# Kernel tuning notes

Hardware: AMD Instinct MI355X
Metric: run time of the kernel (lower is better)

Reference implementation:

```python
import jax, jax.numpy as jnp
import numpy as np

N_NODES = 50000
N_EDGES = 1600000
F_IN = 128
C = 64          # block in/out channels
EF = 64         # edge MLP hidden dim
BLOCKS = 3
MLP_DIM = 128
N_CLASSES = 10
N_GRAPHS = 512
EPS = 1e-5


def setup_inputs() -> dict:
    key = jax.random.key(0)
    ks = jax.random.split(key, 32)
    s = 0.05
    inp = {
        "x": jax.random.normal(ks[0], (N_NODES, F_IN), jnp.float32),
        "edge_index": jax.random.randint(ks[1], (2, N_EDGES), 0, N_NODES, jnp.int64),
        "batch": jnp.sort(jax.random.randint(ks[2], (N_NODES,), 0, N_GRAPHS, jnp.int64)),
        "fc0_w": jax.random.normal(ks[3], (F_IN, C), jnp.float32) * s,
        "fc0_b": jnp.zeros((C,), jnp.float32),
        "fc1_w": jax.random.normal(ks[4], (BLOCKS * C, MLP_DIM), jnp.float32) * s,
        "fc1_b": jnp.zeros((MLP_DIM,), jnp.float32),
        "fc2_w": jax.random.normal(ks[5], (MLP_DIM, N_CLASSES), jnp.float32) * s,
        "fc2_b": jnp.zeros((N_CLASSES,), jnp.float32),
    }
    for i in range(BLOCKS):
        k = 6 + 4 * i
        inp[f"bn_g{i}"] = jnp.ones((C,), jnp.float32)
        inp[f"bn_b{i}"] = jnp.zeros((C,), jnp.float32)
        inp[f"w1_{i}"] = jax.random.normal(ks[k], (2 * C, EF), jnp.float32) * s
        inp[f"b1_{i}"] = jnp.zeros((EF,), jnp.float32)
        inp[f"w2_{i}"] = jax.random.normal(ks[k + 1], (EF, C), jnp.float32) * s
        inp[f"b2_{i}"] = jnp.zeros((C,), jnp.float32)
    return inp


def _batchnorm(x, g, b):
    mu = jnp.mean(x, axis=0)
    var = jnp.var(x, axis=0)
    return (x - mu) * jax.lax.rsqrt(var + EPS) * g + b


def _edge_conv(x, src, dst, w1, b1, w2, b2):
    # PyG-style EdgeConv: msg = MLP(concat[x_i, x_j - x_i]), max-aggregate at i
    xi = x[dst]                                  # [E, C]
    xj = x[src]                                  # [E, C]
    h = jax.nn.relu(jnp.concatenate([xi, xj - xi], axis=-1) @ w1 + b1)  # [E, EF]
    m = h @ w2 + b2                              # [E, C]
    agg = jax.ops.segment_max(m, dst, num_segments=N_NODES)
    return jnp.where(jnp.isfinite(agg), agg, 0.0)


def reference(x, edge_index, batch, fc0_w, fc0_b, fc1_w, fc1_b, fc2_w, fc2_b,
              bn_g0, bn_b0, w1_0, b1_0, w2_0, b2_0,
              bn_g1, bn_b1, w1_1, b1_1, w2_1, b2_1,
              bn_g2, bn_b2, w1_2, b1_2, w2_2, b2_2):
    src, dst = edge_index[0], edge_index[1]
    h = x @ fc0_w + fc0_b                        # [N, C]
    blocks = [(bn_g0, bn_b0, w1_0, b1_0, w2_0, b2_0),
              (bn_g1, bn_b1, w1_1, b1_1, w2_1, b2_1),
              (bn_g2, bn_b2, w1_2, b1_2, w2_2, b2_2)]
    xs = []
    for (g, b, w1, b1, w2, b2) in blocks:
        h = _batchnorm(h, g, b)
        h = jax.nn.relu(_edge_conv(h, src, dst, w1, b1, w2, b2))
        xs.append(h)
    cat = jnp.concatenate(xs, axis=-1)           # [N, 3C]
    # global mean pool over graphs
    sums = jax.ops.segment_sum(cat, batch, num_segments=N_GRAPHS)
    cnt = jax.ops.segment_sum(jnp.ones((N_NODES,), cat.dtype), batch,
                              num_segments=N_GRAPHS)
    pooled = sums / jnp.maximum(cnt, 1.0)[:, None]   # [G, 3C]
    hid = jax.nn.relu(pooled @ fc1_w + fc1_b)
    return jax.nn.log_softmax(hid @ fc2_w + fc2_b, axis=-1)
```

## Files before the change

kernel.cpp:

```cpp
#include <hip/hip_runtime.h>
#include <math.h>

#define N_NODES 50000
#define N_TILES 3125
#define N_EDGES 1600000
#define F_IN 128
#define C 64
#define EF 64
#define N_GRAPHS 512
#define MLP_DIM 128
#define N_CLASSES 10
#define EPS 1e-5f
#define NB 196
#define CAPB 16384
#define CHUNK 4096
#define NPASS1 391
#define NFC0 782
#define NSLICE 8

typedef __attribute__((ext_vector_type(8))) _Float16 half8;
typedef __attribute__((ext_vector_type(2))) _Float16 half2v;
typedef __attribute__((ext_vector_type(4))) float floatx4;
typedef __attribute__((ext_vector_type(4))) unsigned uintx4;

union Uh { uintx4 v; half2v h[4]; half8 h8; };

__device__ __forceinline__ unsigned short f2h(float a) {
    union { _Float16 f; unsigned short u; } c;
    c.f = (_Float16)a;
    return c.u;
}
__device__ __forceinline__ float h2f(unsigned short u) {
    union { unsigned short u; _Float16 f; } c;
    c.u = u;
    return (float)c.f;
}
__device__ __forceinline__ half2v pk2(float a, float b) {
    auto t = __builtin_amdgcn_cvt_pkrtz(a, b);
    union { decltype(t) i; half2v o; } c;
    c.i = t;
    return c.o;
}

__global__ __launch_bounds__(256, 3) void fc0_pass1_kernel(
        const int* __restrict__ src, const int* __restrict__ dst,
        int* __restrict__ gcur, unsigned* __restrict__ keys,
        const float* __restrict__ x, const float* __restrict__ w,
        const float* __restrict__ b, unsigned short* __restrict__ h0,
        float* __restrict__ bns) {
    __shared__ int lcnt[NB], lbase[NB], lcnt2[NB];
    __shared__ float bl1[4][64], bl2[4][64];
    int tid = threadIdx.x;

    if (blockIdx.x < NPASS1) {
        int e0 = blockIdx.x * CHUNK;
        unsigned k[CHUNK / 256];
        int bk[CHUNK / 256];
        for (int i = tid; i < NB; i += 256) lcnt[i] = 0;
        __syncthreads();
#pragma unroll
        for (int i = 0; i < CHUNK / 256; i++) {
            int e = e0 + i * 256 + tid;
            if (e < N_EDGES) {
                int d = dst[e];
                k[i] = ((unsigned)d << 16) | (unsigned)src[e];
                bk[i] = d >> 8;
                atomicAdd(&lcnt[bk[i]], 1);
            } else bk[i] = -1;
        }
        __syncthreads();
        for (int i = tid; i < NB; i += 256) {
            int c = lcnt[i];
            lbase[i] = c ? atomicAdd(&gcur[i], c) : 0;
            lcnt2[i] = 0;
        }
        __syncthreads();
#pragma unroll
        for (int i = 0; i < CHUNK / 256; i++) {
            if (bk[i] >= 0) {
                int r = atomicAdd(&lcnt2[bk[i]], 1);
                keys[(size_t)bk[i] * CAPB + lbase[bk[i]] + r] = k[i];
            }
        }
        return;
    }

    int bid = blockIdx.x - NPASS1;
    int lane = tid & 63, wid = tid >> 6;
    int q = lane >> 4, cl = lane & 15, kq = q * 8;

    Uh wf[4][4];
#pragma unroll
    for (int kh = 0; kh < 4; kh++)
#pragma unroll
        for (int cb = 0; cb < 4; cb++)
#pragma unroll
            for (int j = 0; j < 4; j++) {
                int k0 = kh * 32 + kq + 2 * j;
                int col = cb * 16 + cl;
                wf[kh][cb].h[j] = pk2(w[k0 * 64 + col], w[(k0 + 1) * 64 + col]);
            }
    float bv[4];
#pragma unroll
    for (int cb = 0; cb < 4; cb++) bv[cb] = b[cb * 16 + cl];
    float s1[4] = {0, 0, 0, 0}, s2[4] = {0, 0, 0, 0};

    for (int t = bid * 4 + wid; t < N_TILES; t += NFC0 * 4) {
        int nb = t * 16;
        floatx4 acc[4] = {{0,0,0,0},{0,0,0,0},{0,0,0,0},{0,0,0,0}};
#pragma unroll
        for (int kh = 0; kh < 4; kh++) {
            const float* xr = x + (size_t)(nb + cl) * F_IN + kh * 32 + kq;
            floatx4 xa = *(const floatx4*)xr;
            floatx4 xb = *(const floatx4*)(xr + 4);
            Uh xf;
            xf.h[0] = pk2(xa.x, xa.y); xf.h[1] = pk2(xa.z, xa.w);
            xf.h[2] = pk2(xb.x, xb.y); xf.h[3] = pk2(xb.z, xb.w);
#pragma unroll
            for (int cb = 0; cb < 4; cb++)
                acc[cb] = __builtin_amdgcn_mfma_f32_16x16x32_f16(xf.h8, wf[kh][cb].h8, acc[cb], 0, 0, 0);
        }
#pragma unroll
        for (int cb = 0; cb < 4; cb++)
#pragma unroll
            for (int r = 0; r < 4; r++) {
                float v = acc[cb][r] + bv[cb];
                h0[(size_t)(nb + q * 4 + r) * 64 + cb * 16 + cl] = f2h(v);
                s1[cb] += v; s2[cb] += v * v;
            }
    }
#pragma unroll
    for (int cb = 0; cb < 4; cb++) {
        s1[cb] += __shfl_xor(s1[cb], 16); s1[cb] += __shfl_xor(s1[cb], 32);
        s2[cb] += __shfl_xor(s2[cb], 16); s2[cb] += __shfl_xor(s2[cb], 32);
    }
    if (lane < 16) {
#pragma unroll
        for (int cb = 0; cb < 4; cb++) { bl1[wid][cb * 16 + lane] = s1[cb]; bl2[wid][cb * 16 + lane] = s2[cb]; }
    }
    __syncthreads();
    if (tid < 64) {
        float a  = bl1[0][tid] + bl1[1][tid] + bl1[2][tid] + bl1[3][tid];
        float c2 = bl2[0][tid] + bl2[1][tid] + bl2[2][tid] + bl2[3][tid];
        int sl = bid & (NSLICE - 1);
        atomicAdd(&bns[sl * 128 + tid], a);
        atomicAdd(&bns[sl * 128 + 64 + tid], c2);
    }
}

__device__ __forceinline__ void ab_body(int bid, int tid,
                                        const unsigned short* __restrict__ h,
                                        const float* __restrict__ bns,
                                        const float* __restrict__ g,
                                        const float* __restrict__ bb,
                                        const float* __restrict__ w1,
                                        const float* __restrict__ b1,
                                        unsigned short* __restrict__ A,
                                        unsigned short* __restrict__ Bb,
                                        float* scale, float* shift, float* cab) {
    int lane = tid & 63, wid = tid >> 6;
    int q = lane >> 4, cl = lane & 15, kq = q * 8;

    if (tid < 64) {
        float s1v = 0.f, s2v = 0.f;
#pragma unroll
        for (int s = 0; s < NSLICE; s++) { s1v += bns[s * 128 + tid]; s2v += bns[s * 128 + 64 + tid]; }
        float mu  = s1v * (1.0f / N_NODES);
        float var = s2v * (1.0f / N_NODES) - mu * mu;
        float sc  = g[tid] * rsqrtf(var + EPS);
        scale[tid] = sc;
        shift[tid] = bb[tid] - mu * sc;
    }
    __syncthreads();
    if (tid < 128) {
        int j = tid & 63;
        float acc = (tid < 64) ? b1[j] : 0.f;
        for (int k = 0; k < 64; k++) {
            float wa_ = w1[k * EF + j], wb_ = w1[(64 + k) * EF + j];
            acc = fmaf(shift[k], (tid < 64) ? (wa_ - wb_) : wb_, acc);
        }
        cab[tid] = acc;
    }
    Uh wa[2][4], wb[2][4];
#pragma unroll
    for (int kh = 0; kh < 2; kh++)
#pragma unroll
        for (int cb = 0; cb < 4; cb++)
#pragma unroll
            for (int j = 0; j < 4; j++) {
                int k0 = kh * 32 + kq + 2 * j;
                int col = cb * 16 + cl;
                float sa = scale[k0], sb = scale[k0 + 1];
                float a0 = w1[k0 * EF + col], b0 = w1[(64 + k0) * EF + col];
                float a1 = w1[(k0 + 1) * EF + col], b1v = w1[(64 + k0 + 1) * EF + col];
                wa[kh][cb].h[j] = pk2(sa * (a0 - b0), sb * (a1 - b1v));
                wb[kh][cb].h[j] = pk2(sa * b0, sb * b1v);
            }
    __syncthreads();
    float cav[4], cbv[4];
#pragma unroll
    for (int cb = 0; cb < 4; cb++) { cav[cb] = cab[cb * 16 + cl]; cbv[cb] = cab[64 + cb * 16 + cl]; }

    for (int t = bid * 4 + wid; t < N_TILES; t += NFC0 * 4) {
        int nb = t * 16;
        const unsigned short* hrow = h + (size_t)(nb + cl) * 64 + kq;
        Uh h0f, h1f;
        h0f.v = *(const uintx4*)hrow;
        h1f.v = *(const uintx4*)(hrow + 32);
        floatx4 accA[4] = {{0,0,0,0},{0,0,0,0},{0,0,0,0},{0,0,0,0}};
        floatx4 accB[4] = {{0,0,0,0},{0,0,0,0},{0,0,0,0},{0,0,0,0}};
#pragma unroll
        for (int cb = 0; cb < 4; cb++) {
            accA[cb] = __builtin_amdgcn_mfma_f32_16x16x32_f16(h0f.h8, wa[0][cb].h8, accA[cb], 0, 0, 0);
            accB[cb] = __builtin_amdgcn_mfma_f32_16x16x32_f16(h0f.h8, wb[0][cb].h8, accB[cb], 0, 0, 0);
            accA[cb] = __builtin_amdgcn_mfma_f32_16x16x32_f16(h1f.h8, wa[1][cb].h8, accA[cb], 0, 0, 0);
            accB[cb] = __builtin_amdgcn_mfma_f32_16x16x32_f16(h1f.h8, wb[1][cb].h8, accB[cb], 0, 0, 0);
        }
#pragma unroll
        for (int cb = 0; cb < 4; cb++)
#pragma unroll
            for (int r = 0; r < 4; r++) {
                size_t o = (size_t)(nb + q * 4 + r) * 64 + cb * 16 + cl;
                A[o]  = f2h(accA[cb][r] + cav[cb]);
                Bb[o] = f2h(accB[cb][r] + cbv[cb]);
            }
    }
}

__global__ __launch_bounds__(256, 4) void sort2_ab_kernel(
        const unsigned* __restrict__ keys, const int* __restrict__ bcnt,
        int* __restrict__ cnt, int* __restrict__ gtotal,
        int* __restrict__ row_start, unsigned short* __restrict__ sorted_src,
        const unsigned short* __restrict__ h, const float* __restrict__ bns,
        const float* __restrict__ g, const float* __restrict__ bb,
        const float* __restrict__ w1, const float* __restrict__ b1,
        unsigned short* __restrict__ A, unsigned short* __restrict__ Bb) {
    __shared__ int lc[256], loc[256], rs[256], cur[256];
    __shared__ int base;
    __shared__ float scale[64], shift[64], cab[128];
    int tid = threadIdx.x;
    if (blockIdx.x < NB) {
        int b = blockIdx.x;
        lc[tid] = 0;
        cur[tid] = 0;
        __syncthreads();
        int beg = b * CAPB, end = beg + bcnt[b];
        const unsigned* kb = keys + beg;
        int nk = end - beg;
        for (int p = tid; p < nk; p += 256)
            atomicAdd(&lc[(kb[p] >> 16) & 255], 1);
        __syncthreads();
        int node = b * 256 + tid;
        int c = lc[tid];
        if (node < N_NODES) cnt[node] = c;
        int pc = (c + 15) & ~15;
        loc[tid] = pc;
        __syncthreads();
        for (int off = 1; off < 256; off <<= 1) {
            int t = (tid >= off) ? loc[tid - off] : 0;
            __syncthreads();
            loc[tid] += t;
            __syncthreads();
        }
        if (tid == 255) base = atomicAdd(gtotal, loc[255]);
        __syncthreads();
        int myrs = base + loc[tid] - pc;
        rs[tid] = myrs;
        if (node < N_NODES) row_start[node] = myrs;
        __syncthreads();
        for (int p = tid; p < nk; p += 256) {
            unsigned k = kb[p];
            int lidx = (k >> 16) & 255;
            int r = atomicAdd(&cur[lidx], 1);
            sorted_src[rs[lidx] + r] = (unsigned short)(k & 0xFFFFu);
        }
        __syncthreads();
        if (node < N_NODES && c > 0) {
            unsigned short s0 = sorted_src[myrs];
            int pe = myrs + pc;
            for (int p = myrs + c; p < pe; p++) sorted_src[p] = s0;
        }
        return;
    }
    ab_body(blockIdx.x - NB, tid, h, bns, g, bb, w1, b1, A, Bb, scale, shift, cab);
}

__global__ __launch_bounds__(256, 4) void ab_mfma_kernel(
        const unsigned short* __restrict__ h, const float* __restrict__ bns,
        const float* __restrict__ g, const float* __restrict__ bb,
        const float* __restrict__ w1, const float* __restrict__ b1,
        unsigned short* __restrict__ A, unsigned short* __restrict__ Bb) {
    __shared__ float scale[64], shift[64], cab[128];
    ab_body(blockIdx.x, threadIdx.x, h, bns, g, bb, w1, b1, A, Bb, scale, shift, cab);
}

__global__ __launch_bounds__(256, 4) void edge_mfma_kernel(
        const unsigned short* __restrict__ A, const unsigned short* __restrict__ Bb,
        const int* __restrict__ row_start, const int* __restrict__ cnt,
        const unsigned short* __restrict__ sorted_src,
        const float* __restrict__ w2, const float* __restrict__ b2,
        unsigned short* __restrict__ catp, float* __restrict__ bnsNext) {
    __shared__ float r1[4][64], r2[4][64];
    int tid = threadIdx.x, lane = tid & 63, wid = tid >> 6;
    int kq = (lane >> 4) * 8;
    int cl = lane & 15;

    Uh bfr[2][4];
#pragma unroll
    for (int kh = 0; kh < 2; kh++)
#pragma unroll
        for (int cb = 0; cb < 4; cb++)
#pragma unroll
            for (int j = 0; j < 4; j++) {
                _Float16 w0 = (_Float16)w2[(kh * 32 + kq + 2 * j) * 64 + cb * 16 + cl];
                _Float16 w1 = (_Float16)w2[(kh * 32 + kq + 2 * j + 1) * 64 + cb * 16 + cl];
                bfr[kh][cb].h[j] = half2v{w0, w1};
            }
    float b2j = b2[lane];
    float s1 = 0.f, s2 = 0.f;
    const half2v zeroh = {(_Float16)0.f, (_Float16)0.f};

    for (int n = blockIdx.x * 4 + wid; n < N_NODES; n += gridDim.x * 4) {
        int beg = row_start[n];
        int end = beg + ((cnt[n] + 15) & ~15);
        const unsigned short* arow = A + (size_t)n * 64 + kq;
        Uh a0u, a1u;
        a0u.v = *(const uintx4*)(arow);
        a1u.v = *(const uintx4*)(arow + 32);
        floatx4 rmax0 = {-INFINITY, -INFINITY, -INFINITY, -INFINITY};
        floatx4 rmax1 = rmax0, rmax2 = rmax0, rmax3 = rmax0;

        auto tile = [&](uintx4 u0, uintx4 u1) {
            Uh b0u, b1u, f0, f1;
            b0u.v = u0; b1u.v = u1;
#pragma unroll
            for (int j = 0; j < 4; j++) {
                f0.h[j] = __builtin_elementwise_max(a0u.h[j] + b0u.h[j], zeroh);
                f1.h[j] = __builtin_elementwise_max(a1u.h[j] + b1u.h[j], zeroh);
            }
            floatx4 acc0 = {0.f, 0.f, 0.f, 0.f}, acc1 = acc0, acc2 = acc0, acc3 = acc0;
            acc0 = __builtin_amdgcn_mfma_f32_16x16x32_f16(f0.h8, bfr[0][0].h8, acc0, 0, 0, 0);
            acc1 = __builtin_amdgcn_mfma_f32_16x16x32_f16(f0.h8, bfr[0][1].h8, acc1, 0, 0, 0);
            acc2 = __builtin_amdgcn_mfma_f32_16x16x32_f16(f0.h8, bfr[0][2].h8, acc2, 0, 0, 0);
            acc3 = __builtin_amdgcn_mfma_f32_16x16x32_f16(f0.h8, bfr[0][3].h8, acc3, 0, 0, 0);
            acc0 = __builtin_amdgcn_mfma_f32_16x16x32_f16(f1.h8, bfr[1][0].h8, acc0, 0, 0, 0);
            acc1 = __builtin_amdgcn_mfma_f32_16x16x32_f16(f1.h8, bfr[1][1].h8, acc1, 0, 0, 0);
            acc2 = __builtin_amdgcn_mfma_f32_16x16x32_f16(f1.h8, bfr[1][2].h8, acc2, 0, 0, 0);
            acc3 = __builtin_amdgcn_mfma_f32_16x16x32_f16(f1.h8, bfr[1][3].h8, acc3, 0, 0, 0);
            rmax0 = __builtin_elementwise_max(rmax0, acc0);
            rmax1 = __builtin_elementwise_max(rmax1, acc1);
            rmax2 = __builtin_elementwise_max(rmax2, acc2);
            rmax3 = __builtin_elementwise_max(rmax3, acc3);
        };
        auto gather = [&](int p, uintx4& u0, uintx4& u1) {
            int srcm = sorted_src[p + cl];
            const unsigned short* brow = Bb + (size_t)srcm * 64 + kq;
            u0 = *(const uintx4*)(brow);
            u1 = *(const uintx4*)(brow + 32);
        };

        int p0 = beg;
        for (; p0 + 32 <= end; p0 += 32) {
            uintx4 x0, x1, y0, y1;
            gather(p0, x0, x1);
            gather(p0 + 16, y0, y1);
            tile(x0, x1);
            tile(y0, y1);
        }
        if (p0 < end) {
            uintx4 x0, x1;
            gather(p0, x0, x1);
            tile(x0, x1);
        }

        float v0 = fmaxf(fmaxf(rmax0.x, rmax0.y), fmaxf(rmax0.z, rmax0.w));
        float v1 = fmaxf(fmaxf(rmax1.x, rmax1.y), fmaxf(rmax1.z, rmax1.w));
        float v2 = fmaxf(fmaxf(rmax2.x, rmax2.y), fmaxf(rmax2.z, rmax2.w));
        float v3 = fmaxf(fmaxf(rmax3.x, rmax3.y), fmaxf(rmax3.z, rmax3.w));
        v0 = fmaxf(v0, __shfl_xor(v0, 16)); v0 = fmaxf(v0, __shfl_xor(v0, 32));
        v1 = fmaxf(v1, __shfl_xor(v1, 16)); v1 = fmaxf(v1, __shfl_xor(v1, 32));
        v2 = fmaxf(v2, __shfl_xor(v2, 16)); v2 = fmaxf(v2, __shfl_xor(v2, 32));
        v3 = fmaxf(v3, __shfl_xor(v3, 16)); v3 = fmaxf(v3, __shfl_xor(v3, 32));
        float vs = (lane & 32) ? ((lane & 16) ? v3 : v2) : ((lane & 16) ? v1 : v0);
        float v = fmaxf(vs + b2j, 0.f);
        catp[(size_t)n * 64 + lane] = f2h(v);
        s1 += v; s2 += v * v;
    }

    if (bnsNext) {
        r1[wid][lane] = s1; r2[wid][lane] = s2;
        __syncthreads();
        if (tid < 64) {
            float a  = r1[0][tid] + r1[1][tid] + r1[2][tid] + r1[3][tid];
            float c2 = r2[0][tid] + r2[1][tid] + r2[2][tid] + r2[3][tid];
            int sl = blockIdx.x & (NSLICE - 1);
            atomicAdd(&bnsNext[sl * 128 + tid], a);
            atomicAdd(&bnsNext[sl * 128 + 64 + tid], c2);
        }
    }
}

__global__ __launch_bounds__(192) void poolhead_kernel(const unsigned short* __restrict__ cat0,
                                                       const unsigned short* __restrict__ cat1,
                                                       const unsigned short* __restrict__ cat2,
                                                       const int* __restrict__ batch,
                                                       const float* __restrict__ fc1w,
                                                       const float* __restrict__ fc1b,
                                                       const float* __restrict__ fc2w,
                                                       const float* __restrict__ fc2b,
                                                       float* __restrict__ out) {
    __shared__ int se[2];
    __shared__ float p[192];
    __shared__ float hid[128];
    __shared__ float z[10];
    __shared__ float lse;
    int g = blockIdx.x, tid = threadIdx.x;
    if (tid < 2) {
        int target = g + tid;
        int lo = 0, hi = N_NODES;
        while (lo < hi) { int mid = (lo + hi) >> 1; if (batch[mid] < target) lo = mid + 1; else hi = mid; }
        se[tid] = lo;
    }
    __syncthreads();
    int s = se[0], e = se[1];
    const unsigned short* plane = (tid < 64) ? cat0 : ((tid < 128) ? cat1 : cat2);
    int col = tid & 63;
    float a0 = 0.f, a1 = 0.f, a2 = 0.f, a3 = 0.f;
    int r = s;
    for (; r + 4 <= e; r += 4) {
        a0 += h2f(plane[(size_t)(r + 0) * 64 + col]);
        a1 += h2f(plane[(size_t)(r + 1) * 64 + col]);
        a2 += h2f(plane[(size_t)(r + 2) * 64 + col]);
        a3 += h2f(plane[(size_t)(r + 3) * 64 + col]);
    }
    for (; r < e; r++) a0 += h2f(plane[(size_t)r * 64 + col]);
    float acc = (a0 + a1) + (a2 + a3);
    float denom = (e > s) ? (float)(e - s) : 1.0f;
    p[tid] = acc / denom;
    __syncthreads();
    if (tid < MLP_DIM) {
        float a = fc1b[tid];
        for (int k = 0; k < 192; k++) a = fmaf(p[k], fc1w[k * 128 + tid], a);
        hid[tid] = fmaxf(a, 0.f);
    }
    __syncthreads();
    if (tid < N_CLASSES) {
        float a = fc2b[tid];
        for (int k = 0; k < 128; k++) a = fmaf(hid[k], fc2w[k * 10 + tid], a);
        z[tid] = a;
    }
    __syncthreads();
    if (tid == 0) {
        float m = z[0];
        for (int i = 1; i < 10; i++) m = fmaxf(m, z[i]);
        float sm = 0.f;
        for (int i = 0; i < 10; i++) sm += expf(z[i] - m);
        lse = m + logf(sm);
    }
    __syncthreads();
    if (tid < N_CLASSES) out[g * 10 + tid] = z[tid] - lse;
}

extern "C" void kernel_launch(void* const* d_in, const int* in_sizes, int n_in,
                              void* d_out, int out_size, void* d_ws, size_t ws_size,
                              hipStream_t stream) {
    (void)in_sizes; (void)n_in; (void)out_size; (void)ws_size;
    const float* x    = (const float*)d_in[0];
    const int*   ei   = (const int*)d_in[1];
    const int*   batch= (const int*)d_in[2];
    const float* fc0w = (const float*)d_in[3];
    const float* fc0b = (const float*)d_in[4];
    const float* fc1w = (const float*)d_in[5];
    const float* fc1b = (const float*)d_in[6];
    const float* fc2w = (const float*)d_in[7];
    const float* fc2b = (const float*)d_in[8];
    const int* src = ei;
    const int* dst = ei + N_EDGES;
    float* out = (float*)d_out;

    char* w = (char*)d_ws;
    size_t off = 0;
    auto alloc = [&](size_t bytes) -> void* {
        void* p = w + off;
        off = (off + bytes + 255) & ~(size_t)255;
        return p;
    };
    const size_t MAX_PAD_EDGES = (size_t)N_EDGES + 16 * (size_t)N_NODES;

    const size_t BNS_OFF = 1280;
    const size_t ZBYTES  = BNS_OFF + 3 * NSLICE * 128 * 4;
    char* zbase = (char*)alloc(ZBYTES);
    int*   gcur   = (int*)zbase;
    int*   gtotal = (int*)(zbase + 1024);
    float* bnsAll = (float*)(zbase + BNS_OFF);

    unsigned short* cat0 = (unsigned short*)alloc((size_t)N_NODES * 64 * 2);
    unsigned short* cat1 = (unsigned short*)alloc((size_t)N_NODES * 64 * 2);
    unsigned short* cat2 = (unsigned short*)alloc((size_t)N_NODES * 64 * 2);
    unsigned short* h0   = (unsigned short*)alloc((size_t)N_NODES * 64 * 2);
    unsigned short* Ae   = (unsigned short*)alloc((size_t)N_NODES * 64 * 2);
    unsigned short* Be   = (unsigned short*)alloc((size_t)N_NODES * 64 * 2);
    unsigned* keys = (unsigned*)alloc((size_t)NB * CAPB * 4);
    unsigned short* sorted_src = (unsigned short*)alloc(MAX_PAD_EDGES * 2);
    int*   cnt       = (int*)alloc((size_t)N_NODES * 4);
    int*   row_start = (int*)alloc((size_t)N_NODES * 4);

    (void)hipMemsetAsync(zbase, 0, ZBYTES, stream);

    fc0_pass1_kernel<<<NPASS1 + NFC0, 256, 0, stream>>>(src, dst, gcur, keys,
                                                        x, fc0w, fc0b, h0, bnsAll);
    sort2_ab_kernel<<<NB + NFC0, 256, 0, stream>>>(
        keys, gcur, cnt, gtotal, row_start, sorted_src,
        h0, bnsAll,
        (const float*)d_in[9], (const float*)d_in[10],
        (const float*)d_in[11], (const float*)d_in[12], Ae, Be);

    unsigned short* planes[3] = {cat0, cat1, cat2};
    for (int blk = 0; blk < 3; blk++) {
        const float* w2 = (const float*)d_in[13 + 6 * blk];
        const float* b2 = (const float*)d_in[14 + 6 * blk];
        if (blk > 0) {
            ab_mfma_kernel<<<NFC0, 256, 0, stream>>>(
                planes[blk - 1], bnsAll + blk * NSLICE * 128,
                (const float*)d_in[9 + 6 * blk], (const float*)d_in[10 + 6 * blk],
                (const float*)d_in[11 + 6 * blk], (const float*)d_in[12 + 6 * blk], Ae, Be);
        }
        edge_mfma_kernel<<<2048, 256, 0, stream>>>(
            Ae, Be, row_start, cnt, sorted_src, w2, b2, planes[blk],
            (blk < 2) ? (bnsAll + (blk + 1) * NSLICE * 128) : nullptr);
    }

    poolhead_kernel<<<N_GRAPHS, 192, 0, stream>>>(cat0, cat1, cat2, batch,
                                                  fc1w, fc1b, fc2w, fc2b, out);
}
```

Before: 380.0 us.

## Assign contiguous node ranges per wave and prefetch next node's edge indices

The edge kernel now gives each wave a fixed contiguous range of 6 or 7 nodes instead of a grid-stride loop. It software-pipelines the index loads: the next node's row_start, cnt and first two sorted_src entries are fetched while the current node computes, and the next tile's source index is prefetched inside the loop. This aims to hide the dependent index-then-gather latency chain, at the cost of extra registers and a static split that could leave waves unbalanced when node degrees vary.

Result: slower. 411.1 us (+8.2%).

```diff
diff --git a/kernel.cpp b/kernel.cpp
--- a/kernel.cpp
+++ b/kernel.cpp
@@ -17,6 +17,9 @@
 #define NPASS1 391
 #define NFC0 782
 #define NSLICE 8
+#define EDGE_GRID 2048
+#define N_WAVES 8192
+#define EXTRA_W 848
 
 typedef __attribute__((ext_vector_type(8))) _Float16 half8;
 typedef __attribute__((ext_vector_type(2))) _Float16 half2v;
@@ -313,20 +316,50 @@
 #pragma unroll
             for (int j = 0; j < 4; j++) {
                 _Float16 w0 = (_Float16)w2[(kh * 32 + kq + 2 * j) * 64 + cb * 16 + cl];
-                _Float16 w1 = (_Float16)w2[(kh * 32 + kq + 2 * j + 1) * 64 + cb * 16 + cl];
-                bfr[kh][cb].h[j] = half2v{w0, w1};
+                _Float16 w1v = (_Float16)w2[(kh * 32 + kq + 2 * j + 1) * 64 + cb * 16 + cl];
+                bfr[kh][cb].h[j] = half2v{w0, w1v};
             }
     float b2j = b2[lane];
     float s1 = 0.f, s2 = 0.f;
     const half2v zeroh = {(_Float16)0.f, (_Float16)0.f};
 
-    for (int n = blockIdx.x * 4 + wid; n < N_NODES; n += gridDim.x * 4) {
-        int beg = row_start[n];
-        int end = beg + ((cnt[n] + 15) & ~15);
+    int wv = blockIdx.x * 4 + wid;
+    int n0 = wv * 6 + (wv < EXTRA_W ? wv : EXTRA_W);
+    int nodes = (wv < EXTRA_W) ? 7 : 6;
+
+    int rs = row_start[n0];
+    int ct = cnt[n0];
+    int s0i = (int)sorted_src[rs + cl];
+    int s1i = (int)sorted_src[rs + 16 + cl];
+
+    for (int ni = 0; ni < nodes; ni++) {
+        int n = n0 + ni;
+        int beg = rs, c = ct;
+        int nt = (c + 15) >> 4;
+        int cs0 = s0i, cs1 = s1i;
+        if (ni + 1 < nodes) {
+            rs = row_start[n + 1];
+            ct = cnt[n + 1];
+        }
+
+        int snext = (nt > 2) ? (int)sorted_src[beg + 32 + cl] : 0;
+
+        uintx4 x0, x1, y0, y1;
+        if (nt > 0) {
+            const unsigned short* brow = Bb + (size_t)cs0 * 64 + kq;
+            x0 = *(const uintx4*)(brow);
+            x1 = *(const uintx4*)(brow + 32);
+        }
+        if (nt > 1) {
+            const unsigned short* brow = Bb + (size_t)cs1 * 64 + kq;
+            y0 = *(const uintx4*)(brow);
+            y1 = *(const uintx4*)(brow + 32);
+        }
         const unsigned short* arow = A + (size_t)n * 64 + kq;
         Uh a0u, a1u;
         a0u.v = *(const uintx4*)(arow);
         a1u.v = *(const uintx4*)(arow + 32);
+
         floatx4 rmax0 = {-INFINITY, -INFINITY, -INFINITY, -INFINITY};
         floatx4 rmax1 = rmax0, rmax2 = rmax0, rmax3 = rmax0;
 
@@ -352,25 +385,21 @@
             rmax2 = __builtin_elementwise_max(rmax2, acc2);
             rmax3 = __builtin_elementwise_max(rmax3, acc3);
         };
-        auto gather = [&](int p, uintx4& u0, uintx4& u1) {
-            int srcm = sorted_src[p + cl];
-            const unsigned short* brow = Bb + (size_t)srcm * 64 + kq;
-            u0 = *(const uintx4*)(brow);
-            u1 = *(const uintx4*)(brow + 32);
-        };
-
-        int p0 = beg;
-        for (; p0 + 32 <= end; p0 += 32) {
-            uintx4 x0, x1, y0, y1;
-            gather(p0, x0, x1);
-            gather(p0 + 16, y0, y1);
-            tile(x0, x1);
-            tile(y0, y1);
-        }
-        if (p0 < end) {
-            uintx4 x0, x1;
-            gather(p0, x0, x1);
-            tile(x0, x1);
+
+        if (nt > 0) tile(x0, x1);
+        if (nt > 1) tile(y0, y1);
+        for (int t = 2; t < nt; t++) {
+            int scur = snext;
+            if (t + 1 < nt) snext = (int)sorted_src[beg + (t + 1) * 16 + cl];
+            const unsigned short* brow = Bb + (size_t)scur * 64 + kq;
+            uintx4 u0 = *(const uintx4*)(brow);
+            uintx4 u1 = *(const uintx4*)(brow + 32);
+            tile(u0, u1);
+        }
+
+        if (ni + 1 < nodes) {
+            s0i = (int)sorted_src[rs + cl];
+            s1i = (int)sorted_src[rs + 16 + cl];
         }
 
         float v0 = fmaxf(fmaxf(rmax0.x, rmax0.y), fmaxf(rmax0.z, rmax0.w));
@@ -525,7 +554,7 @@
                 (const float*)d_in[9 + 6 * blk], (const float*)d_in[10 + 6 * blk],
                 (const float*)d_in[11 + 6 * blk], (const float*)d_in[12 + 6 * blk], Ae, Be);
         }
-        edge_mfma_kernel<<<2048, 256, 0, stream>>>(
+        edge_mfma_kernel<<<EDGE_GRID, 256, 0, stream>>>(
             Ae, Be, row_start, cnt, sorted_src, w2, b2, planes[blk],
             (blk < 2) ? (bnsAll + (blk + 1) * NSLICE * 128) : nullptr);
     }
```
